# Performance work log

Hardware: AMD Instinct MI355X
Metric: run time of the kernel (lower is better)

Reference implementation:

```python
import jax, jax.numpy as jnp
import numpy as np

N_NODES = 100000
N_EDGES = 3200000
N_GRAPHS = 64

def setup_inputs() -> dict:
    key = jax.random.key(0)
    ks = jax.random.split(key, 10)
    x = jax.random.normal(ks[0], (N_NODES, 7), dtype=jnp.float32)
    edge_index = jax.random.randint(ks[1], (2, N_EDGES), 0, N_NODES, dtype=jnp.int64)
    batch = jnp.sort(jax.random.randint(ks[2], (N_NODES,), 0, N_GRAPHS, dtype=jnp.int64))
    # Glorot-ish init for weights (values irrelevant for correctness baseline)
    W1 = jax.random.normal(ks[3], (7, 64), dtype=jnp.float32) * 0.3
    b1 = jnp.zeros((64,), dtype=jnp.float32)
    W2 = jax.random.normal(ks[4], (64, 32), dtype=jnp.float32) * 0.12
    b2 = jnp.zeros((32,), dtype=jnp.float32)
    Wl = jax.random.normal(ks[5], (32, 5), dtype=jnp.float32) * 0.17
    bl = jnp.zeros((5,), dtype=jnp.float32)
    return {"x": x, "edge_index": edge_index, "batch": batch,
            "W1": W1, "b1": b1, "W2": W2, "b2": b2, "Wl": Wl, "bl": bl}


def _gcn_conv(x, row, col, W, b, n_nodes):
    """PyG GCNConv: out = D^{-1/2} (A + I) D^{-1/2} X W + b.
    row/col already include self-loops; aggregation at target `col`."""
    h = x @ W                                         # [N, F_out]
    ones = jnp.ones(row.shape[0], dtype=x.dtype)
    deg = jax.ops.segment_sum(ones, col, num_segments=n_nodes)
    dinv = jnp.where(deg > 0, jax.lax.rsqrt(deg), 0.0)
    norm = dinv[row] * dinv[col]                      # [E]
    msg = h[row] * norm[:, None]                      # [E, F_out] gather
    out = jax.ops.segment_sum(msg, col, num_segments=n_nodes)  # scatter-add
    return out + b


def reference(x, edge_index, batch, W1, b1, W2, b2, Wl, bl):
    n = x.shape[0]
    loop = jnp.arange(n, dtype=edge_index.dtype)
    row = jnp.concatenate([edge_index[0], loop])      # add self-loops
    col = jnp.concatenate([edge_index[1], loop])

    h = jax.nn.relu(_gcn_conv(x, row, col, W1, b1, n))
    h = jax.nn.relu(_gcn_conv(h, row, col, W2, b2, n))
    h = h @ Wl + bl                                   # [N, 5]

    # global_mean_pool over graph ids
    sums = jax.ops.segment_sum(h, batch, num_segments=N_GRAPHS)
    cnts = jax.ops.segment_sum(jnp.ones((n,), h.dtype), batch, num_segments=N_GRAPHS)
    return sums / jnp.maximum(cnts, 1.0)[:, None]
```

## Files before the change

kernel.cpp:

```cpp
#include <hip/hip_runtime.h>

#define N_GRAPHS 64
#define EPB 8192
#define BSTAGE 16384
#define SROWSTRIDE 16384

#if __has_builtin(__builtin_amdgcn_cvt_pk_f32_fp8) && __has_builtin(__builtin_amdgcn_cvt_pk_fp8_f32)
#define HAS_FP8 1
#else
#define HAS_FP8 0
#endif

typedef float f32x2 __attribute__((ext_vector_type(2)));

__device__ inline float bf2f(unsigned short u) {
    union { unsigned u; float f; } c; c.u = (unsigned)u << 16; return c.f;
}
__device__ inline unsigned short f2bf(float f) {
    union { float f; unsigned u; } c; c.f = f;
    unsigned b = c.u;
    return (unsigned short)((b + 0x7fffu + ((b >> 16) & 1u)) >> 16);
}

__global__ __launch_bounds__(256) void k_count2(
        const int* __restrict__ row, const int* __restrict__ col,
        int* __restrict__ meta, unsigned int* __restrict__ ebuf,
        int E, int NBLK, int NBK) {
    __shared__ int h[512];
    __shared__ int scn[512];
    __shared__ unsigned recs[EPB];
    __shared__ unsigned short bucks[EPB];
    int t = threadIdx.x;
    int i0 = t, i1 = t + 256;
    h[i0] = 0; h[i1] = 0;
    __syncthreads();
    int s = blockIdx.x * EPB, e = min(E, s + EPB);
    int m = e - s;
    int nvec = m >> 2;
    const uint4* col4 = (const uint4*)(col + s);
    const uint4* row4 = (const uint4*)(row + s);
    for (int v = t; v < nvec; v += 256) {
        uint4 c = col4[v];
        uint4 r = row4[v];
        int j = v << 2;
        recs[j + 0] = (r.x << 8) | (c.x & 255u); bucks[j + 0] = (unsigned short)(c.x >> 8);
        recs[j + 1] = (r.y << 8) | (c.y & 255u); bucks[j + 1] = (unsigned short)(c.y >> 8);
        recs[j + 2] = (r.z << 8) | (c.z & 255u); bucks[j + 2] = (unsigned short)(c.z >> 8);
        recs[j + 3] = (r.w << 8) | (c.w & 255u); bucks[j + 3] = (unsigned short)(c.w >> 8);
        atomicAdd(&h[c.x >> 8], 1);
        atomicAdd(&h[c.y >> 8], 1);
        atomicAdd(&h[c.z >> 8], 1);
        atomicAdd(&h[c.w >> 8], 1);
    }
    for (int j = (nvec << 2) + t; j < m; j += 256) {
        unsigned c = (unsigned)col[s + j], r = (unsigned)row[s + j];
        recs[j] = (r << 8) | (c & 255u);
        bucks[j] = (unsigned short)(c >> 8);
        atomicAdd(&h[c >> 8], 1);
    }
    __syncthreads();
    scn[i0] = h[i0]; scn[i1] = h[i1];
    __syncthreads();
    for (int d = 1; d < 512; d <<= 1) {
        int v0 = (i0 >= d) ? scn[i0 - d] : 0;
        int v1 = (i1 >= d) ? scn[i1 - d] : 0;
        __syncthreads();
        scn[i0] += v0; scn[i1] += v1;
        __syncthreads();
    }
    int* mrow = meta + (size_t)blockIdx.x * NBK;
    if (i0 < NBK) { int c0 = h[i0], l0 = scn[i0] - c0; mrow[i0] = (l0 << 16) | c0; }
    if (i1 < NBK) { int c1 = h[i1], l1 = scn[i1] - c1; mrow[i1] = (l1 << 16) | c1; }
    __syncthreads();
    h[i0] = s + scn[i0] - h[i0];
    h[i1] = s + scn[i1] - h[i1];
    __syncthreads();
    for (int j = t; j < m; j += 256) {
        int p = atomicAdd(&h[bucks[j]], 1);
        ebuf[p] = recs[j];
    }
}

__global__ __launch_bounds__(256) void k_bprep(
        const unsigned int* __restrict__ ebuf, const int* __restrict__ meta,
        const float* __restrict__ x,
        float* __restrict__ dinv, unsigned short* __restrict__ xs,
        int* __restrict__ off, int* __restrict__ oend, int* __restrict__ srow,
        int n, int NBLK, int NBK) {
    __shared__ int h[256];
    __shared__ int cur[256];
    __shared__ int cnts[512];
    __shared__ int locs[512];
    __shared__ int scn[512];
    __shared__ unsigned stage[BSTAGE];
    int t = threadIdx.x, b = blockIdx.x;
    int i0 = t, i1 = t + 256;
    h[t] = 0;
    cnts[i0] = 0; cnts[i1] = 0;
    __syncthreads();
    for (int k = t; k < NBLK; k += 256) {
        int m = meta[(size_t)k * NBK + b];
        cnts[k] = m & 0xffff;
        locs[k] = m >> 16;
    }
    __syncthreads();
    scn[i0] = cnts[i0]; scn[i1] = cnts[i1];
    __syncthreads();
    for (int d = 1; d < 512; d <<= 1) {
        int v0 = (i0 >= d) ? scn[i0 - d] : 0;
        int v1 = (i1 >= d) ? scn[i1 - d] : 0;
        __syncthreads();
        scn[i0] += v0; scn[i1] += v1;
        __syncthreads();
    }
    int mtot = scn[511];
    bool fit = (mtot <= BSTAGE);
    if (fit) {
        for (int k = t; k < NBLK; k += 256) {
            int cnt = cnts[k];
            const unsigned* src = ebuf + (size_t)k * EPB + locs[k];
            int dst = scn[k] - cnt;
            for (int q = 0; q < cnt; q++) {
                unsigned rec = src[q];
                stage[dst + q] = rec;
                atomicAdd(&h[rec & 255], 1);
            }
        }
    } else {
        for (int k = t; k < NBLK; k += 256) {
            int cnt = cnts[k];
            const unsigned* src = ebuf + (size_t)k * EPB + locs[k];
            for (int q = 0; q < cnt; q++)
                atomicAdd(&h[src[q] & 255], 1);
        }
    }
    __syncthreads();
    int dg = h[t];
    cur[t] = dg;
    __syncthreads();
    for (int d = 1; d < 256; d <<= 1) {
        int tmp = (t >= d) ? cur[t - d] : 0;
        __syncthreads();
        cur[t] += tmp;
        __syncthreads();
    }
    int base = b * SROWSTRIDE;
    int myoff = base + cur[t] - dg;
    int node = b * 256 + t;
    if (node < n) {
        off[node]  = myoff;
        oend[node] = myoff + dg;
        float d = rsqrtf((float)(dg + 1));
        dinv[node] = d;
        unsigned short r[8];
#pragma unroll
        for (int k = 0; k < 7; k++) r[k] = f2bf(x[(size_t)node * 7 + k] * d);
        r[7] = 0;
        uint4 v;
        v.x = (unsigned)r[0] | ((unsigned)r[1] << 16);
        v.y = (unsigned)r[2] | ((unsigned)r[3] << 16);
        v.z = (unsigned)r[4] | ((unsigned)r[5] << 16);
        v.w = (unsigned)r[6] | ((unsigned)r[7] << 16);
        *(uint4*)(xs + (size_t)node * 8) = v;
    }
    __syncthreads();
    cur[t] = myoff;
    __syncthreads();
    if (fit) {
        for (int j = t; j < mtot; j += 256) {
            unsigned rec = stage[j];
            int p = atomicAdd(&cur[rec & 255], 1);
            srow[p] = (int)(rec >> 8);
        }
    } else {
        for (int k = t; k < NBLK; k += 256) {
            int cnt = cnts[k];
            const unsigned* src = ebuf + (size_t)k * EPB + locs[k];
            for (int q = 0; q < cnt; q++) {
                unsigned rec = src[q];
                int p = atomicAdd(&cur[rec & 255], 1);
                srow[p] = (int)(rec >> 8);
            }
        }
    }
}

__global__ __launch_bounds__(256) void k_agg1(
        const unsigned short* __restrict__ xs, const float* __restrict__ dinv,
        const int* __restrict__ off, const int* __restrict__ oend,
        const int* __restrict__ srow, float* __restrict__ aggx, int n) {
    int tid = blockIdx.x * blockDim.x + threadIdx.x;
    int c = tid >> 2;
    if (c >= n) return;
    int fp = tid & 3;
    int o0 = off[c], o1 = oend[c];
    f32x2 A = {0.f, 0.f};
    auto addp = [&](unsigned u) {
        union { unsigned x; float f; } lo, hi;
        lo.x = u << 16;
        hi.x = u & 0xffff0000u;
        f32x2 v; v.x = lo.f; v.y = hi.f;
        A += v;
    };
    addp(*(const unsigned*)(xs + (size_t)c * 8 + fp * 2));
    int j = o0;
    for (; j + 4 <= o1; j += 4) {
        int r0 = srow[j], r1 = srow[j + 1], r2 = srow[j + 2], r3 = srow[j + 3];
        unsigned u0 = *(const unsigned*)(xs + (size_t)r0 * 8 + fp * 2);
        unsigned u1 = *(const unsigned*)(xs + (size_t)r1 * 8 + fp * 2);
        unsigned u2 = *(const unsigned*)(xs + (size_t)r2 * 8 + fp * 2);
        unsigned u3 = *(const unsigned*)(xs + (size_t)r3 * 8 + fp * 2);
        addp(u0); addp(u1); addp(u2); addp(u3);
    }
    for (; j < o1; j++)
        addp(*(const unsigned*)(xs + (size_t)srow[j] * 8 + fp * 2));
    float d = dinv[c];
    aggx[(size_t)c * 8 + fp * 2]     = A.x * d;
    aggx[(size_t)c * 8 + fp * 2 + 1] = A.y * d;
}

__global__ __launch_bounds__(256) void k_mlp1(
        const float* __restrict__ aggx, const float* __restrict__ dinv,
        const float* __restrict__ W1, const float* __restrict__ b1,
        const float* __restrict__ W2,
        unsigned int* __restrict__ hs,
        const int* __restrict__ batch, int* __restrict__ gstart, int n) {
    __shared__ float sW1[7 * 64];
    __shared__ float sb1[64];
    __shared__ float sW2[64 * 32];
    for (int t = threadIdx.x; t < 7 * 64; t += blockDim.x) sW1[t] = W1[t];
    for (int t = threadIdx.x; t < 64; t += blockDim.x) sb1[t] = b1[t];
    for (int t = threadIdx.x; t < 64 * 32; t += blockDim.x) sW2[t] = W2[t];
    __syncthreads();

    int i = blockIdx.x * blockDim.x + threadIdx.x;
    if (i >= n) return;

    {
        int g = batch[i];
        int gp = (i == 0) ? -1 : batch[i - 1];
        for (int q = gp + 1; q <= g; q++) gstart[q] = i;
        if (i == n - 1)
            for (int q = g + 1; q <= N_GRAPHS; q++) gstart[q] = n;
    }

    float a[7];
#pragma unroll
    for (int k = 0; k < 7; k++) a[k] = aggx[(size_t)i * 8 + k];

    float acc[32];
#pragma unroll
    for (int m = 0; m < 32; m++) acc[m] = 0.f;

    for (int j = 0; j < 64; j++) {
        float v = sb1[j];
#pragma unroll
        for (int k = 0; k < 7; k++) v += a[k] * sW1[k * 64 + j];
        v = fmaxf(v, 0.f);
#pragma unroll
        for (int m = 0; m < 32; m++) acc[m] += v * sW2[j * 32 + m];
    }
    float d = dinv[i];
#if HAS_FP8
    float sc = d * 8.f;
    unsigned w[8];
#pragma unroll
    for (int q = 0; q < 8; q++) {
        unsigned t0 = (unsigned)__builtin_amdgcn_cvt_pk_fp8_f32(
            acc[4 * q] * sc, acc[4 * q + 1] * sc, 0, false);
        w[q] = (unsigned)__builtin_amdgcn_cvt_pk_fp8_f32(
            acc[4 * q + 2] * sc, acc[4 * q + 3] * sc, (int)t0, true);
    }
    uint4* o = (uint4*)(hs + (size_t)i * 8);
    o[0] = make_uint4(w[0], w[1], w[2], w[3]);
    o[1] = make_uint4(w[4], w[5], w[6], w[7]);
#else
    unsigned up[16];
#pragma unroll
    for (int m = 0; m < 16; m++)
        up[m] = (unsigned)f2bf(acc[2 * m] * d) |
                ((unsigned)f2bf(acc[2 * m + 1] * d) << 16);
    uint4* o = (uint4*)(hs + (size_t)i * 16);
    o[0] = make_uint4(up[0],  up[1],  up[2],  up[3]);
    o[1] = make_uint4(up[4],  up[5],  up[6],  up[7]);
    o[2] = make_uint4(up[8],  up[9],  up[10], up[11]);
    o[3] = make_uint4(up[12], up[13], up[14], up[15]);
#endif
}

__global__ __launch_bounds__(256) void k_agg2(
        const unsigned int* __restrict__ hs, const float* __restrict__ dinv,
        const int* __restrict__ off, const int* __restrict__ oend,
        const int* __restrict__ srow, float* __restrict__ agg2, int n) {
    int tid = blockIdx.x * blockDim.x + threadIdx.x;
    int c = tid >> 2;
    if (c >= n) return;
    int fp = tid & 3;
    int o0 = off[c], o1 = oend[c];
#if HAS_FP8
    f32x2 A0 = {0.f, 0.f}, A1 = {0.f, 0.f}, A2 = {0.f, 0.f}, A3 = {0.f, 0.f};
    auto dec = [&](uint2 u) {
        A0 += __builtin_amdgcn_cvt_pk_f32_fp8((int)u.x, false);
        A1 += __builtin_amdgcn_cvt_pk_f32_fp8((int)u.x, true);
        A2 += __builtin_amdgcn_cvt_pk_f32_fp8((int)u.y, false);
        A3 += __builtin_amdgcn_cvt_pk_f32_fp8((int)u.y, true);
    };
    dec(*(const uint2*)(hs + (size_t)c * 8 + fp * 2));
    int j = o0;
    for (; j + 4 <= o1; j += 4) {
        int r0 = srow[j], r1 = srow[j + 1], r2 = srow[j + 2], r3 = srow[j + 3];
        uint2 u0 = *(const uint2*)(hs + (size_t)r0 * 8 + fp * 2);
        uint2 u1 = *(const uint2*)(hs + (size_t)r1 * 8 + fp * 2);
        uint2 u2 = *(const uint2*)(hs + (size_t)r2 * 8 + fp * 2);
        uint2 u3 = *(const uint2*)(hs + (size_t)r3 * 8 + fp * 2);
        dec(u0); dec(u1); dec(u2); dec(u3);
    }
    for (; j < o1; j++)
        dec(*(const uint2*)(hs + (size_t)srow[j] * 8 + fp * 2));
    float d = dinv[c] * 0.125f;
    float4* o = (float4*)(agg2 + (size_t)c * 32 + fp * 8);
    o[0] = make_float4(A0.x * d, A0.y * d, A1.x * d, A1.y * d);
    o[1] = make_float4(A2.x * d, A2.y * d, A3.x * d, A3.y * d);
#else
    float a0 = 0.f, a1 = 0.f, a2 = 0.f, a3 = 0.f;
    float a4 = 0.f, a5 = 0.f, a6 = 0.f, a7 = 0.f;
    auto addpair = [&](float& x0, float& x1, unsigned u) {
        union { unsigned x; float f; } lo, hi;
        lo.x = u << 16; hi.x = u & 0xffff0000u;
        x0 += lo.f; x1 += hi.f;
    };
    auto dec = [&](uint4 u) {
        addpair(a0, a1, u.x); addpair(a2, a3, u.y);
        addpair(a4, a5, u.z); addpair(a6, a7, u.w);
    };
    dec(*(const uint4*)(hs + (size_t)c * 16 + fp * 4));
    int j = o0;
    for (; j + 4 <= o1; j += 4) {
        int r0 = srow[j], r1 = srow[j + 1], r2 = srow[j + 2], r3 = srow[j + 3];
        uint4 u0 = *(const uint4*)(hs + (size_t)r0 * 16 + fp * 4);
        uint4 u1 = *(const uint4*)(hs + (size_t)r1 * 16 + fp * 4);
        uint4 u2 = *(const uint4*)(hs + (size_t)r2 * 16 + fp * 4);
        uint4 u3 = *(const uint4*)(hs + (size_t)r3 * 16 + fp * 4);
        dec(u0); dec(u1); dec(u2); dec(u3);
    }
    for (; j < o1; j++)
        dec(*(const uint4*)(hs + (size_t)srow[j] * 16 + fp * 4));
    float d = dinv[c];
    float4* o = (float4*)(agg2 + (size_t)c * 32 + fp * 8);
    o[0] = make_float4(a0 * d, a1 * d, a2 * d, a3 * d);
    o[1] = make_float4(a4 * d, a5 * d, a6 * d, a7 * d);
#endif
}

__global__ __launch_bounds__(256) void k_pool(
        const float* __restrict__ agg2, const float* __restrict__ b2,
        const int* __restrict__ gstart, float* __restrict__ psum) {
    int g = blockIdx.x >> 3, ch = blockIdx.x & 7;
    int s = gstart[g], e = gstart[g + 1];
    int cnt = e - s;
    int per = (cnt + 7) >> 3;
    int cs = s + ch * per, ce = min(e, cs + per);

    int t = threadIdx.x;
    int fq = t & 7, nl = t >> 3;
    const float4* b2q4 = (const float4*)b2;
    float4 bq = b2q4[fq];
    float4 acc = make_float4(0.f, 0.f, 0.f, 0.f);
    for (int i = cs + nl; i < ce; i += 32) {
        float4 v = *(const float4*)(agg2 + (size_t)i * 32 + fq * 4);
        acc.x += fmaxf(v.x + bq.x, 0.f);
        acc.y += fmaxf(v.y + bq.y, 0.f);
        acc.z += fmaxf(v.z + bq.z, 0.f);
        acc.w += fmaxf(v.w + bq.w, 0.f);
    }
#pragma unroll
    for (int m = 8; m < 64; m <<= 1) {
        acc.x += __shfl_xor(acc.x, m);
        acc.y += __shfl_xor(acc.y, m);
        acc.z += __shfl_xor(acc.z, m);
        acc.w += __shfl_xor(acc.w, m);
    }
    __shared__ float4 part[4][8];
    int w = t >> 6, lane = t & 63;
    if (lane < 8) part[w][lane] = acc;
    __syncthreads();
    if (t < 8) {
        float4 p0 = part[0][t], p1 = part[1][t], p2 = part[2][t], p3 = part[3][t];
        float4 r;
        r.x = p0.x + p1.x + p2.x + p3.x;
        r.y = p0.y + p1.y + p2.y + p3.y;
        r.z = p0.z + p1.z + p2.z + p3.z;
        r.w = p0.w + p1.w + p2.w + p3.w;
        *(float4*)(psum + ((size_t)((g << 3) + ch)) * 32 + t * 4) = r;
    }
}

__global__ void k_out(const float* __restrict__ psum, const int* __restrict__ gstart,
                      const float* __restrict__ Wl, const float* __restrict__ bl,
                      float* __restrict__ out) {
    int t = blockIdx.x * blockDim.x + threadIdx.x;
    if (t >= N_GRAPHS * 5) return;
    int g = t / 5, o = t % 5;
    float c = (float)max(gstart[g + 1] - gstart[g], 1);
    float acc = 0.f;
#pragma unroll
    for (int m = 0; m < 32; m++) {
        float s = 0.f;
#pragma unroll
        for (int ch = 0; ch < 8; ch++)
            s += psum[((size_t)((g << 3) + ch)) * 32 + m];
        acc += s * Wl[m * 5 + o];
    }
    out[t] = acc / c + bl[o];
}

extern "C" void kernel_launch(void* const* d_in, const int* in_sizes, int n_in,
                              void* d_out, int out_size, void* d_ws, size_t ws_size,
                              hipStream_t stream) {
    const float* x     = (const float*)d_in[0];
    const int*   ei    = (const int*)d_in[1];
    const int*   batch = (const int*)d_in[2];
    const float* W1    = (const float*)d_in[3];
    const float* b1    = (const float*)d_in[4];
    const float* W2    = (const float*)d_in[5];
    const float* b2    = (const float*)d_in[6];
    const float* Wl    = (const float*)d_in[7];
    const float* bl    = (const float*)d_in[8];
    float* out = (float*)d_out;

    const int n = in_sizes[0] / 7;
    const int E = in_sizes[1] / 2;
    const int* row = ei;
    const int* col = ei + E;

    const int NBK  = (n + 255) >> 8;
    const int NBLK = (E + EPB - 1) / EPB;

    char* p = (char*)d_ws;
    auto alloc = [&](size_t bytes) -> char* {
        char* r = p;
        p += (bytes + 255) & ~(size_t)255;
        return r;
    };
    int*   meta   = (int*)  alloc((size_t)NBLK * NBK * 4);
    unsigned int* ebuf = (unsigned int*)alloc((size_t)E * 4);
    int*   srow   = (int*)  alloc((size_t)NBK * SROWSTRIDE * 4);
    float* dinv   = (float*)alloc((size_t)n * 4);
    int*   off    = (int*)  alloc((size_t)n * 4);
    int*   oendv  = (int*)  alloc((size_t)n * 4);
    unsigned short* xs = (unsigned short*)alloc((size_t)n * 8 * 2);
    float* aggx   = (float*)alloc((size_t)n * 8 * 4);
    unsigned int* hs = (unsigned int*)alloc((size_t)n * 16 * 4);
    float* agg2   = (float*)alloc((size_t)n * 32 * 4);
    int*   gstart = (int*)  alloc((N_GRAPHS + 1) * 4);
    float* psum   = (float*)alloc((size_t)N_GRAPHS * 8 * 32 * 4);

    const int BT = 256;
    int nb_n    = (n + BT - 1) / BT;
    int nb_quad = (n * 4 + BT - 1) / BT;

    k_count2 <<<NBLK, BT, 0, stream>>>(row, col, meta, ebuf, E, NBLK, NBK);
    k_bprep  <<<NBK, BT, 0, stream>>>(ebuf, meta, x, dinv, xs, off, oendv, srow,
                                      n, NBLK, NBK);

    k_agg1   <<<nb_quad, BT, 0, stream>>>(xs, dinv, off, oendv, srow, aggx, n);
    k_mlp1   <<<nb_n, BT, 0, stream>>>(aggx, dinv, W1, b1, W2, hs, batch, gstart, n);
    k_agg2   <<<nb_quad, BT, 0, stream>>>(hs, dinv, off, oendv, srow, agg2, n);
    k_pool   <<<N_GRAPHS * 8, BT, 0, stream>>>(agg2, b2, gstart, psum);
    k_out    <<<1, 320, 0, stream>>>(psum, gstart, Wl, bl, out);
}
```

Before: 142.0 us.

## Fuse second-layer aggregation with bias, ReLU and per-graph mean pooling

Merges the layer-2 neighbour aggregation kernel with the pooling kernel. Each block now walks a chunk of one graph's nodes, aggregates their neighbours, applies bias and ReLU in registers, and reduces into per-chunk partial sums, so the [N,32] agg2 buffer is never written or read back. The grid shrinks from one quad of threads per node to 64x24 blocks. That can reduce parallelism and latency hiding for the gather-heavy loop, and k_out now sums 24 partials per graph.

```diff
diff --git a/kernel.cpp b/kernel.cpp
--- a/kernel.cpp
+++ b/kernel.cpp
@@ -4,6 +4,7 @@
 #define EPB 8192
 #define BSTAGE 16384
 #define SROWSTRIDE 16384
+#define PCHUNK 24
 
 #if __has_builtin(__builtin_amdgcn_cvt_pk_f32_fp8) && __has_builtin(__builtin_amdgcn_cvt_pk_fp8_f32)
 #define HAS_FP8 1
@@ -288,110 +289,106 @@
 #endif
 }
 
-__global__ __launch_bounds__(256) void k_agg2(
+__global__ __launch_bounds__(256) void k_agg2p(
         const unsigned int* __restrict__ hs, const float* __restrict__ dinv,
         const int* __restrict__ off, const int* __restrict__ oend,
-        const int* __restrict__ srow, float* __restrict__ agg2, int n) {
-    int tid = blockIdx.x * blockDim.x + threadIdx.x;
-    int c = tid >> 2;
-    if (c >= n) return;
-    int fp = tid & 3;
-    int o0 = off[c], o1 = oend[c];
+        const int* __restrict__ srow, const int* __restrict__ gstart,
+        const float* __restrict__ b2, float* __restrict__ psum, int n) {
+    int g = blockIdx.x / PCHUNK, ch = blockIdx.x % PCHUNK;
+    int gs = gstart[g], ge = gstart[g + 1];
+    int cnt = ge - gs;
+    int per = (cnt + PCHUNK - 1) / PCHUNK;
+    int cs = gs + ch * per, ce = min(ge, cs + per);
+
+    int t = threadIdx.x;
+    int q = t >> 2, fp = t & 3;
+    float4 bq0 = *(const float4*)(b2 + fp * 8);
+    float4 bq1 = *(const float4*)(b2 + fp * 8 + 4);
+    f32x2 P0 = {0.f, 0.f}, P1 = {0.f, 0.f}, P2 = {0.f, 0.f}, P3 = {0.f, 0.f};
+
+    for (int c = cs + q; c < ce; c += 64) {
+        int o0 = off[c], o1 = oend[c];
 #if HAS_FP8
-    f32x2 A0 = {0.f, 0.f}, A1 = {0.f, 0.f}, A2 = {0.f, 0.f}, A3 = {0.f, 0.f};
-    auto dec = [&](uint2 u) {
-        A0 += __builtin_amdgcn_cvt_pk_f32_fp8((int)u.x, false);
-        A1 += __builtin_amdgcn_cvt_pk_f32_fp8((int)u.x, true);
-        A2 += __builtin_amdgcn_cvt_pk_f32_fp8((int)u.y, false);
-        A3 += __builtin_amdgcn_cvt_pk_f32_fp8((int)u.y, true);
-    };
-    dec(*(const uint2*)(hs + (size_t)c * 8 + fp * 2));
-    int j = o0;
-    for (; j + 4 <= o1; j += 4) {
-        int r0 = srow[j], r1 = srow[j + 1], r2 = srow[j + 2], r3 = srow[j + 3];
-        uint2 u0 = *(const uint2*)(hs + (size_t)r0 * 8 + fp * 2);
-        uint2 u1 = *(const uint2*)(hs + (size_t)r1 * 8 + fp * 2);
-        uint2 u2 = *(const uint2*)(hs + (size_t)r2 * 8 + fp * 2);
-        uint2 u3 = *(const uint2*)(hs + (size_t)r3 * 8 + fp * 2);
-        dec(u0); dec(u1); dec(u2); dec(u3);
-    }
-    for (; j < o1; j++)
-        dec(*(const uint2*)(hs + (size_t)srow[j] * 8 + fp * 2));
-    float d = dinv[c] * 0.125f;
-    float4* o = (float4*)(agg2 + (size_t)c * 32 + fp * 8);
-    o[0] = make_float4(A0.x * d, A0.y * d, A1.x * d, A1.y * d);
-    o[1] = make_float4(A2.x * d, A2.y * d, A3.x * d, A3.y * d);
+        f32x2 A0 = {0.f, 0.f}, A1 = {0.f, 0.f}, A2 = {0.f, 0.f}, A3 = {0.f, 0.f};
+        auto dec = [&](uint2 u) {
+            A0 += __builtin_amdgcn_cvt_pk_f32_fp8((int)u.x, false);
+            A1 += __builtin_amdgcn_cvt_pk_f32_fp8((int)u.x, true);
+            A2 += __builtin_amdgcn_cvt_pk_f32_fp8((int)u.y, false);
+            A3 += __builtin_amdgcn_cvt_pk_f32_fp8((int)u.y, true);
+        };
+        dec(*(const uint2*)(hs + (size_t)c * 8 + fp * 2));
+        int j = o0;
+        for (; j + 4 <= o1; j += 4) {
+            int r0 = srow[j], r1 = srow[j + 1], r2 = srow[j + 2], r3 = srow[j + 3];
+            uint2 u0 = *(const uint2*)(hs + (size_t)r0 * 8 + fp * 2);
+            uint2 u1 = *(const uint2*)(hs + (size_t)r1 * 8 + fp * 2);
+            uint2 u2 = *(const uint2*)(hs + (size_t)r2 * 8 + fp * 2);
+            uint2 u3 = *(const uint2*)(hs + (size_t)r3 * 8 + fp * 2);
+            dec(u0); dec(u1); dec(u2); dec(u3);
+        }
+        for (; j < o1; j++)
+            dec(*(const uint2*)(hs + (size_t)srow[j] * 8 + fp * 2));
+        float d = dinv[c] * 0.125f;
 #else
-    float a0 = 0.f, a1 = 0.f, a2 = 0.f, a3 = 0.f;
-    float a4 = 0.f, a5 = 0.f, a6 = 0.f, a7 = 0.f;
-    auto addpair = [&](float& x0, float& x1, unsigned u) {
-        union { unsigned x; float f; } lo, hi;
-        lo.x = u << 16; hi.x = u & 0xffff0000u;
-        x0 += lo.f; x1 += hi.f;
-    };
-    auto dec = [&](uint4 u) {
-        addpair(a0, a1, u.x); addpair(a2, a3, u.y);
-        addpair(a4, a5, u.z); addpair(a6, a7, u.w);
-    };
-    dec(*(const uint4*)(hs + (size_t)c * 16 + fp * 4));
-    int j = o0;
-    for (; j + 4 <= o1; j += 4) {
-        int r0 = srow[j], r1 = srow[j + 1], r2 = srow[j + 2], r3 = srow[j + 3];
-        uint4 u0 = *(const uint4*)(hs + (size_t)r0 * 16 + fp * 4);
-        uint4 u1 = *(const uint4*)(hs + (size_t)r1 * 16 + fp * 4);
-        uint4 u2 = *(const uint4*)(hs + (size_t)r2 * 16 + fp * 4);
-        uint4 u3 = *(const uint4*)(hs + (size_t)r3 * 16 + fp * 4);
-        dec(u0); dec(u1); dec(u2); dec(u3);
-    }
-    for (; j < o1; j++)
-        dec(*(const uint4*)(hs + (size_t)srow[j] * 16 + fp * 4));
-    float d = dinv[c];
-    float4* o = (float4*)(agg2 + (size_t)c * 32 + fp * 8);
-    o[0] = make_float4(a0 * d, a1 * d, a2 * d, a3 * d);
-    o[1] = make_float4(a4 * d, a5 * d, a6 * d, a7 * d);
+        f32x2 A0 = {0.f, 0.f}, A1 = {0.f, 0.f}, A2 = {0.f, 0.f}, A3 = {0.f, 0.f};
+        auto addpair = [&](f32x2& X, unsigned u) {
+            union { unsigned x; float f; } lo, hi;
+            lo.x = u << 16; hi.x = u & 0xffff0000u;
+            f32x2 v; v.x = lo.f; v.y = hi.f;
+            X += v;
+        };
+        auto dec = [&](uint4 u) {
+            addpair(A0, u.x); addpair(A1, u.y);
+            addpair(A2, u.z); addpair(A3, u.w);
+        };
+        dec(*(const uint4*)(hs + (size_t)c * 16 + fp * 4));
+        int j = o0;
+        for (; j + 4 <= o1; j += 4) {
+            int r0 = srow[j], r1 = srow[j + 1], r2 = srow[j + 2], r3 = srow[j + 3];
+            uint4 u0 = *(const uint4*)(hs + (size_t)r0 * 16 + fp * 4);
+            uint4 u1 = *(const uint4*)(hs + (size_t)r1 * 16 + fp * 4);
+            uint4 u2 = *(const uint4*)(hs + (size_t)r2 * 16 + fp * 4);
+            uint4 u3 = *(const uint4*)(hs + (size_t)r3 * 16 + fp * 4);
+            dec(u0); dec(u1); dec(u2); dec(u3);
+        }
+        for (; j < o1; j++)
+            dec(*(const uint4*)(hs + (size_t)srow[j] * 16 + fp * 4));
+        float d = dinv[c];
 #endif
-}
-
-__global__ __launch_bounds__(256) void k_pool(
-        const float* __restrict__ agg2, const float* __restrict__ b2,
-        const int* __restrict__ gstart, float* __restrict__ psum) {
-    int g = blockIdx.x >> 3, ch = blockIdx.x & 7;
-    int s = gstart[g], e = gstart[g + 1];
-    int cnt = e - s;
-    int per = (cnt + 7) >> 3;
-    int cs = s + ch * per, ce = min(e, cs + per);
-
-    int t = threadIdx.x;
-    int fq = t & 7, nl = t >> 3;
-    const float4* b2q4 = (const float4*)b2;
-    float4 bq = b2q4[fq];
-    float4 acc = make_float4(0.f, 0.f, 0.f, 0.f);
-    for (int i = cs + nl; i < ce; i += 32) {
-        float4 v = *(const float4*)(agg2 + (size_t)i * 32 + fq * 4);
-        acc.x += fmaxf(v.x + bq.x, 0.f);
-        acc.y += fmaxf(v.y + bq.y, 0.f);
-        acc.z += fmaxf(v.z + bq.z, 0.f);
-        acc.w += fmaxf(v.w + bq.w, 0.f);
-    }
-#pragma unroll
-    for (int m = 8; m < 64; m <<= 1) {
-        acc.x += __shfl_xor(acc.x, m);
-        acc.y += __shfl_xor(acc.y, m);
-        acc.z += __shfl_xor(acc.z, m);
-        acc.w += __shfl_xor(acc.w, m);
-    }
-    __shared__ float4 part[4][8];
+        P0.x += fmaxf(A0.x * d + bq0.x, 0.f);
+        P0.y += fmaxf(A0.y * d + bq0.y, 0.f);
+        P1.x += fmaxf(A1.x * d + bq0.z, 0.f);
+        P1.y += fmaxf(A1.y * d + bq0.w, 0.f);
+        P2.x += fmaxf(A2.x * d + bq1.x, 0.f);
+        P2.y += fmaxf(A2.y * d + bq1.y, 0.f);
+        P3.x += fmaxf(A3.x * d + bq1.z, 0.f);
+        P3.y += fmaxf(A3.y * d + bq1.w, 0.f);
+    }
+
+#pragma unroll
+    for (int m = 4; m < 64; m <<= 1) {
+        P0.x += __shfl_xor(P0.x, m); P0.y += __shfl_xor(P0.y, m);
+        P1.x += __shfl_xor(P1.x, m); P1.y += __shfl_xor(P1.y, m);
+        P2.x += __shfl_xor(P2.x, m); P2.y += __shfl_xor(P2.y, m);
+        P3.x += __shfl_xor(P3.x, m); P3.y += __shfl_xor(P3.y, m);
+    }
+    __shared__ float4 part[4][4][2];
     int w = t >> 6, lane = t & 63;
-    if (lane < 8) part[w][lane] = acc;
+    if (lane < 4) {
+        part[w][lane][0] = make_float4(P0.x, P0.y, P1.x, P1.y);
+        part[w][lane][1] = make_float4(P2.x, P2.y, P3.x, P3.y);
+    }
     __syncthreads();
     if (t < 8) {
-        float4 p0 = part[0][t], p1 = part[1][t], p2 = part[2][t], p3 = part[3][t];
+        int f = t & 3, hf = t >> 2;
+        float4 s0 = part[0][f][hf], s1 = part[1][f][hf];
+        float4 s2 = part[2][f][hf], s3 = part[3][f][hf];
         float4 r;
-        r.x = p0.x + p1.x + p2.x + p3.x;
-        r.y = p0.y + p1.y + p2.y + p3.y;
-        r.z = p0.z + p1.z + p2.z + p3.z;
-        r.w = p0.w + p1.w + p2.w + p3.w;
-        *(float4*)(psum + ((size_t)((g << 3) + ch)) * 32 + t * 4) = r;
+        r.x = s0.x + s1.x + s2.x + s3.x;
+        r.y = s0.y + s1.y + s2.y + s3.y;
+        r.z = s0.z + s1.z + s2.z + s3.z;
+        r.w = s0.w + s1.w + s2.w + s3.w;
+        *(float4*)(psum + ((size_t)(g * PCHUNK + ch)) * 32 + f * 8 + hf * 4) = r;
     }
 }
 
@@ -406,9 +403,8 @@
 #pragma unroll
     for (int m = 0; m < 32; m++) {
         float s = 0.f;
-#pragma unroll
-        for (int ch = 0; ch < 8; ch++)
-            s += psum[((size_t)((g << 3) + ch)) * 32 + m];
+        for (int ch = 0; ch < PCHUNK; ch++)
+            s += psum[((size_t)(g * PCHUNK + ch)) * 32 + m];
         acc += s * Wl[m * 5 + o];
     }
     out[t] = acc / c + bl[o];
@@ -451,9 +447,8 @@
     unsigned short* xs = (unsigned short*)alloc((size_t)n * 8 * 2);
     float* aggx   = (float*)alloc((size_t)n * 8 * 4);
     unsigned int* hs = (unsigned int*)alloc((size_t)n * 16 * 4);
-    float* agg2   = (float*)alloc((size_t)n * 32 * 4);
     int*   gstart = (int*)  alloc((N_GRAPHS + 1) * 4);
-    float* psum   = (float*)alloc((size_t)N_GRAPHS * 8 * 32 * 4);
+    float* psum   = (float*)alloc((size_t)N_GRAPHS * PCHUNK * 32 * 4);
 
     const int BT = 256;
     int nb_n    = (n + BT - 1) / BT;
@@ -465,7 +460,7 @@
 
     k_agg1   <<<nb_quad, BT, 0, stream>>>(xs, dinv, off, oendv, srow, aggx, n);
     k_mlp1   <<<nb_n, BT, 0, stream>>>(aggx, dinv, W1, b1, W2, hs, batch, gstart, n);
-    k_agg2   <<<nb_quad, BT, 0, stream>>>(hs, dinv, off, oendv, srow, agg2, n);
-    k_pool   <<<N_GRAPHS * 8, BT, 0, stream>>>(agg2, b2, gstart, psum);
+    k_agg2p  <<<N_GRAPHS * PCHUNK, BT, 0, stream>>>(hs, dinv, off, oendv, srow,
+                                                    gstart, b2, psum, n);
     k_out    <<<1, 320, 0, stream>>>(psum, gstart, Wl, bl, out);
 }
```

Result: slower. 147.7 us (+4.0%).
